# Kernel optimization log

Measured on AMD Instinct MI355X. Metric: run time of the kernel, lower is better.

The kernel has to match this reference:

```python
import jax, jax.numpy as jnp
import numpy as np

N = 50000
E = 800000
IN_FEATS = 128
OUT_FEATS = 16
EDGE_FEATS = 1
NUM_HEADS = 8


def setup_inputs() -> dict:
    key = jax.random.key(0)
    ks = jax.random.split(key, 8)

    def xavier(k, shape):
        fan_in, fan_out = shape[-1], shape[-2] if len(shape) > 1 else shape[-1]
        bound = float(np.sqrt(6.0 / (shape[0] + shape[1])))
        return jax.random.uniform(k, shape, jnp.float32, -bound, bound)

    h = jax.random.normal(ks[0], (N, IN_FEATS), jnp.float32)
    edge_index = jax.random.randint(ks[1], (2, E), 0, N, jnp.int32)
    edge_feat = jax.random.normal(ks[2], (E, EDGE_FEATS), jnp.float32)
    # W_node stored as [in_feats, out_feats*num_heads] so h @ W_node == torch Linear(h)
    W_node = xavier(ks[3], (IN_FEATS, OUT_FEATS * NUM_HEADS))
    W_edge = xavier(ks[4], (EDGE_FEATS, NUM_HEADS))
    a_src = xavier(ks[5], (NUM_HEADS, OUT_FEATS))
    a_dst = xavier(ks[6], (NUM_HEADS, OUT_FEATS))
    return {"h": h, "edge_index": edge_index, "edge_feat": edge_feat,
            "W_node": W_node, "W_edge": W_edge, "a_src": a_src, "a_dst": a_dst}


def reference(h, edge_index, edge_feat, W_node, W_edge, a_src, a_dst):
    n = h.shape[0]
    src, dst = edge_index[0], edge_index[1]
    # node projection: [N, H, F]
    h_trans = (h @ W_node).reshape(n, NUM_HEADS, OUT_FEATS)
    # edge projection: [E, H]
    e_trans = edge_feat @ W_edge
    src_feat = h_trans[src]  # [E, H, F]
    dst_feat = h_trans[dst]  # [E, H, F]
    attn = (src_feat * a_src).sum(-1) + (dst_feat * a_dst).sum(-1) + e_trans  # [E, H]
    attn = jax.nn.leaky_relu(attn, negative_slope=0.2)
    # segment softmax over edges grouped by dst
    max_val = jax.ops.segment_max(attn, dst, num_segments=n)  # [N, H]
    exp_attn = jnp.exp(attn - max_val[dst])
    sum_exp = jax.ops.segment_sum(exp_attn, dst, num_segments=n)  # [N, H]
    alpha = exp_attn / jnp.maximum(sum_exp[dst], 1e-12)  # [E, H]
    msg = src_feat * alpha[..., None]  # [E, H, F]
    out = jax.ops.segment_sum(msg, dst, num_segments=n)  # [N, H, F]
    return out.mean(axis=1)  # [N, F]
```

## Files before the change

### kernel.cpp

```cpp
#include <hip/hip_runtime.h>

#define N_NODES 50000
#define N_EDGES 800000
#define IN_F    128
#define HEADS   8
#define OUT_F   16

typedef unsigned short u16;
typedef __attribute__((ext_vector_type(8))) short bf16x8;
typedef __attribute__((ext_vector_type(4))) float f32x4;

__device__ __forceinline__ float bf2f(u16 u) {
    return __uint_as_float(((unsigned)u) << 16);
}
__device__ __forceinline__ u16 f2bf(float f) {
    unsigned u = __float_as_uint(f);
    unsigned r = 0x7fffu + ((u >> 16) & 1u);
    return (u16)((u + r) >> 16);
}
__device__ __forceinline__ float ldf(const void* p, int i, bool bf) {
    return bf ? bf2f(((const u16*)p)[i]) : ((const float*)p)[i];
}

__global__ void probe_dtype(const void* __restrict__ h, int* __restrict__ flag) {
    if (threadIdx.x == 0 && blockIdx.x == 0) {
        const u16* u = (const u16*)h;
        int cnt = 0;
        for (int i = 0; i < 128; ++i) {
            int e = (u[i] >> 7) & 0xFF;
            if (e >= 90 && e <= 141) cnt++;
        }
        *flag = (cnt >= 110) ? 1 : 0;
    }
}

__global__ __launch_bounds__(256) void init_bufs(float* __restrict__ sum_exp,
                                                 float* __restrict__ out_acc) {
    int i = blockIdx.x * 256 + threadIdx.x;
    if (i < N_NODES * HEADS)  sum_exp[i] = 0.0f;
    if (i < N_NODES * OUT_F)  out_acc[i] = 0.0f;
}

#define WT_STRIDE 136
__global__ __launch_bounds__(256) void node_proj_mfma(
    const void* __restrict__ h, const void* __restrict__ Wn,
    const void* __restrict__ a_srcp, const void* __restrict__ a_dstp,
    const int* __restrict__ flag,
    u16* __restrict__ ht, float* __restrict__ s_src, float* __restrict__ s_dst)
{
    const bool bf = (*flag) != 0;
    __shared__ u16 Wsh[IN_F * WT_STRIDE];
    const int tid = threadIdx.x;

    for (int i = tid; i < IN_F * IN_F; i += 256) {
        int k = i >> 7, c = i & 127;
        u16 v = bf ? ((const u16*)Wn)[i] : f2bf(((const float*)Wn)[i]);
        Wsh[c * WT_STRIDE + k] = v;
    }
    __syncthreads();

    const int wave = tid >> 6, lane = tid & 63;
    const int m = lane & 15, q = lane >> 4;
    const int row_t = blockIdx.x * 64 + wave * 16;

    bf16x8 afr[4];
    int arow = row_t + m;
    if (arow >= N_NODES) arow = N_NODES - 1;
    if (bf) {
        const u16* hp = (const u16*)h + (size_t)arow * IN_F;
        #pragma unroll
        for (int kt = 0; kt < 4; ++kt)
            afr[kt] = *(const bf16x8*)(hp + kt * 32 + q * 8);
    } else {
        const float* hp = (const float*)h + (size_t)arow * IN_F;
        #pragma unroll
        for (int kt = 0; kt < 4; ++kt) {
            bf16x8 t;
            #pragma unroll
            for (int j = 0; j < 8; ++j) t[j] = (short)f2bf(hp[kt * 32 + q * 8 + j]);
            afr[kt] = t;
        }
    }

    for (int ct = 0; ct < 8; ++ct) {
        f32x4 acc = {0.f, 0.f, 0.f, 0.f};
        #pragma unroll
        for (int kt = 0; kt < 4; ++kt) {
            bf16x8 bfr = *(const bf16x8*)(Wsh + (ct * 16 + m) * WT_STRIDE + kt * 32 + q * 8);
            acc = __builtin_amdgcn_mfma_f32_16x16x32_bf16(afr[kt], bfr, acc, 0, 0, 0);
        }
        const float asv = ldf(a_srcp, ct * 16 + m, bf);
        const float adv = ldf(a_dstp, ct * 16 + m, bf);
        float v1[4], v2[4];
        #pragma unroll
        for (int r = 0; r < 4; ++r) {
            int grow = row_t + q * 4 + r;
            if (grow < N_NODES)
                ht[(size_t)grow * IN_F + ct * 16 + m] = f2bf(acc[r]);
            v1[r] = acc[r] * asv;
            v2[r] = acc[r] * adv;
        }
        #pragma unroll
        for (int o = 1; o < 16; o <<= 1) {
            #pragma unroll
            for (int r = 0; r < 4; ++r) {
                v1[r] += __shfl_xor(v1[r], o, 16);
                v2[r] += __shfl_xor(v2[r], o, 16);
            }
        }
        if (m == 0) {
            #pragma unroll
            for (int r = 0; r < 4; ++r) {
                int grow = row_t + q * 4 + r;
                if (grow < N_NODES) {
                    s_src[grow * HEADS + ct] = v1[r];
                    s_dst[grow * HEADS + ct] = v2[r];
                }
            }
        }
    }
}

__device__ __forceinline__ float edge_attn(const int* ei, const void* ef,
                                           const void* We,
                                           const float* s_src, const float* s_dst,
                                           int e, int hh, bool bf,
                                           int& src, int& dst) {
    src = ei[e];
    dst = ei[N_EDGES + e];
    float a = s_src[src * HEADS + hh] + s_dst[dst * HEADS + hh]
            + ldf(ef, e, bf) * ldf(We, hh, bf);
    return (a > 0.0f) ? a : 0.2f * a;
}

__global__ __launch_bounds__(256) void edge_sum(
    const int* __restrict__ ei, const void* __restrict__ ef,
    const void* __restrict__ We, const int* __restrict__ flag,
    const float* __restrict__ s_src, const float* __restrict__ s_dst,
    float* __restrict__ sum_exp)
{
    const bool bf = (*flag) != 0;
    int t = blockIdx.x * 256 + threadIdx.x;
    if (t >= N_EDGES * HEADS) return;
    int e = t >> 3, hh = t & 7, src, dst;
    float a = edge_attn(ei, ef, We, s_src, s_dst, e, hh, bf, src, dst);
    atomicAdd(&sum_exp[dst * HEADS + hh], __expf(a));
}

__global__ __launch_bounds__(256) void edge_aggregate(
    const int* __restrict__ ei, const void* __restrict__ ef,
    const void* __restrict__ We, const int* __restrict__ flag,
    const float* __restrict__ s_src, const float* __restrict__ s_dst,
    const float* __restrict__ sum_exp,
    const u16* __restrict__ ht, float* __restrict__ out_acc)
{
    const bool bf = (*flag) != 0;
    int t = blockIdx.x * 256 + threadIdx.x;
    int e = t >> 4;
    if (e >= N_EDGES) return;
    int lane = threadIdx.x & 15;
    int hh = lane & 7, src, dst;
    float a = edge_attn(ei, ef, We, s_src, s_dst, e, hh, bf, src, dst);
    float alpha = __expf(a) / fmaxf(sum_exp[dst * HEADS + hh], 1e-12f);

    const u16* hp = ht + (size_t)src * IN_F + lane;
    float acc = 0.0f;
    #pragma unroll
    for (int h2 = 0; h2 < HEADS; ++h2) {
        float ah = __shfl(alpha, h2, 16);
        acc = fmaf(ah, bf2f(hp[h2 * 16]), acc);
    }
    atomicAdd(&out_acc[dst * OUT_F + lane], acc * 0.125f);
}

__global__ __launch_bounds__(256) void finalize(const float* __restrict__ out_acc,
                                                void* __restrict__ out,
                                                const int* __restrict__ flag) {
    const bool bf = (*flag) != 0;
    int i = blockIdx.x * 256 + threadIdx.x;
    if (i < N_NODES * OUT_F) {
        float v = out_acc[i];
        if (bf) ((u16*)out)[i] = f2bf(v);
        else    ((float*)out)[i] = v;
    }
}

extern "C" void kernel_launch(void* const* d_in, const int* in_sizes, int n_in,
                              void* d_out, int out_size, void* d_ws, size_t ws_size,
                              hipStream_t stream) {
    const void* h     = d_in[0];
    const int*  ei    = (const int*)d_in[1];
    const void* efeat = d_in[2];
    const void* Wn    = d_in[3];
    const void* We    = d_in[4];
    const void* a_src = d_in[5];
    const void* a_dst = d_in[6];

    char* ws = (char*)d_ws;
    int*   flag    = (int*)ws;   ws += 256;
    u16*   ht      = (u16*)ws;   ws += (size_t)N_NODES * IN_F * 2;
    float* s_src   = (float*)ws; ws += (size_t)N_NODES * HEADS * 4;
    float* s_dst   = (float*)ws; ws += (size_t)N_NODES * HEADS * 4;
    float* sum_exp = (float*)ws; ws += (size_t)N_NODES * HEADS * 4;
    float* out_acc = (float*)ws; ws += (size_t)N_NODES * OUT_F * 4;

    hipLaunchKernelGGL(probe_dtype, dim3(1), dim3(64), 0, stream, h, flag);
    hipLaunchKernelGGL(init_bufs, dim3((N_NODES * OUT_F + 255) / 256), dim3(256),
                       0, stream, sum_exp, out_acc);
    hipLaunchKernelGGL(node_proj_mfma, dim3((N_NODES + 63) / 64), dim3(256),
                       0, stream, h, Wn, a_src, a_dst, flag, ht, s_src, s_dst);
    hipLaunchKernelGGL(edge_sum, dim3((N_EDGES * HEADS + 255) / 256), dim3(256),
                       0, stream, ei, efeat, We, flag, s_src, s_dst, sum_exp);
    hipLaunchKernelGGL(edge_aggregate, dim3((N_EDGES * 16 + 255) / 256), dim3(256),
                       0, stream, ei, efeat, We, flag, s_src, s_dst, sum_exp,
                       ht, out_acc);
    hipLaunchKernelGGL(finalize, dim3((N_NODES * OUT_F + 255) / 256), dim3(256),
                       0, stream, out_acc, d_out, flag);
}
```

Baseline: 225.1 us.

## Transpose ht layout to feature-major for vectorized loads; one thread per edge in edge_sum

The projected node features are now stored per row with the 8 heads of each output feature packed together (index f*8+head), written as one 16-byte vector per row. edge_aggregate then reads a single 16-byte vector per lane instead of eight strided 2-byte loads. edge_sum assigns one thread per edge, loading the src/dst scores with float4 and issuing eight atomics, instead of one thread per (edge, head). This cuts the number of gather transactions and repeated index loads, but edge_sum now has fewer threads, each doing serialized atomics.

```diff
diff --git a/kernel.cpp b/kernel.cpp
--- a/kernel.cpp
+++ b/kernel.cpp
@@ -82,6 +82,8 @@
         }
     }
 
+    f32x4 accs[8];
+    #pragma unroll
     for (int ct = 0; ct < 8; ++ct) {
         f32x4 acc = {0.f, 0.f, 0.f, 0.f};
         #pragma unroll
@@ -89,14 +91,12 @@
             bf16x8 bfr = *(const bf16x8*)(Wsh + (ct * 16 + m) * WT_STRIDE + kt * 32 + q * 8);
             acc = __builtin_amdgcn_mfma_f32_16x16x32_bf16(afr[kt], bfr, acc, 0, 0, 0);
         }
+        accs[ct] = acc;
         const float asv = ldf(a_srcp, ct * 16 + m, bf);
         const float adv = ldf(a_dstp, ct * 16 + m, bf);
         float v1[4], v2[4];
         #pragma unroll
         for (int r = 0; r < 4; ++r) {
-            int grow = row_t + q * 4 + r;
-            if (grow < N_NODES)
-                ht[(size_t)grow * IN_F + ct * 16 + m] = f2bf(acc[r]);
             v1[r] = acc[r] * asv;
             v2[r] = acc[r] * adv;
         }
@@ -119,18 +119,17 @@
             }
         }
     }
-}
-
-__device__ __forceinline__ float edge_attn(const int* ei, const void* ef,
-                                           const void* We,
-                                           const float* s_src, const float* s_dst,
-                                           int e, int hh, bool bf,
-                                           int& src, int& dst) {
-    src = ei[e];
-    dst = ei[N_EDGES + e];
-    float a = s_src[src * HEADS + hh] + s_dst[dst * HEADS + hh]
-            + ldf(ef, e, bf) * ldf(We, hh, bf);
-    return (a > 0.0f) ? a : 0.2f * a;
+
+    #pragma unroll
+    for (int r = 0; r < 4; ++r) {
+        int grow = row_t + q * 4 + r;
+        if (grow < N_NODES) {
+            bf16x8 o;
+            #pragma unroll
+            for (int ct = 0; ct < 8; ++ct) o[ct] = (short)f2bf(accs[ct][r]);
+            *(bf16x8*)(ht + (size_t)grow * IN_F + m * 8) = o;
+        }
+    }
 }
 
 __global__ __launch_bounds__(256) void edge_sum(
@@ -140,11 +139,24 @@
     float* __restrict__ sum_exp)
 {
     const bool bf = (*flag) != 0;
-    int t = blockIdx.x * 256 + threadIdx.x;
-    if (t >= N_EDGES * HEADS) return;
-    int e = t >> 3, hh = t & 7, src, dst;
-    float a = edge_attn(ei, ef, We, s_src, s_dst, e, hh, bf, src, dst);
-    atomicAdd(&sum_exp[dst * HEADS + hh], __expf(a));
+    int e = blockIdx.x * 256 + threadIdx.x;
+    if (e >= N_EDGES) return;
+    int src = ei[e];
+    int dst = ei[N_EDGES + e];
+    const float4* sp = (const float4*)(s_src + src * HEADS);
+    const float4* dp = (const float4*)(s_dst + dst * HEADS);
+    float4 sa = sp[0], sb = sp[1];
+    float4 da = dp[0], db = dp[1];
+    float efv = ldf(ef, e, bf);
+    float s8[8] = {sa.x, sa.y, sa.z, sa.w, sb.x, sb.y, sb.z, sb.w};
+    float d8[8] = {da.x, da.y, da.z, da.w, db.x, db.y, db.z, db.w};
+    float* se = sum_exp + dst * HEADS;
+    #pragma unroll
+    for (int hh = 0; hh < 8; ++hh) {
+        float a = s8[hh] + d8[hh] + efv * ldf(We, hh, bf);
+        a = (a > 0.0f) ? a : 0.2f * a;
+        atomicAdd(&se[hh], __expf(a));
+    }
 }
 
 __global__ __launch_bounds__(256) void edge_aggregate(
@@ -159,16 +171,23 @@
     int e = t >> 4;
     if (e >= N_EDGES) return;
     int lane = threadIdx.x & 15;
-    int hh = lane & 7, src, dst;
-    float a = edge_attn(ei, ef, We, s_src, s_dst, e, hh, bf, src, dst);
-    float alpha = __expf(a) / fmaxf(sum_exp[dst * HEADS + hh], 1e-12f);
-
-    const u16* hp = ht + (size_t)src * IN_F + lane;
+    int src = ei[e];
+    int dst = ei[N_EDGES + e];
+
+    float alpha = 0.0f;
+    if (lane < 8) {
+        float a = s_src[src * HEADS + lane] + s_dst[dst * HEADS + lane]
+                + ldf(ef, e, bf) * ldf(We, lane, bf);
+        a = (a > 0.0f) ? a : 0.2f * a;
+        alpha = __expf(a) / fmaxf(sum_exp[dst * HEADS + lane], 1e-12f);
+    }
+
+    bf16x8 v = *(const bf16x8*)(ht + (size_t)src * IN_F + lane * 8);
     float acc = 0.0f;
     #pragma unroll
     for (int h2 = 0; h2 < HEADS; ++h2) {
         float ah = __shfl(alpha, h2, 16);
-        acc = fmaf(ah, bf2f(hp[h2 * 16]), acc);
+        acc = fmaf(ah, bf2f((u16)v[h2]), acc);
     }
     atomicAdd(&out_acc[dst * OUT_F + lane], acc * 0.125f);
 }
@@ -209,7 +228,7 @@
                        0, stream, sum_exp, out_acc);
     hipLaunchKernelGGL(node_proj_mfma, dim3((N_NODES + 63) / 64), dim3(256),
                        0, stream, h, Wn, a_src, a_dst, flag, ht, s_src, s_dst);
-    hipLaunchKernelGGL(edge_sum, dim3((N_EDGES * HEADS + 255) / 256), dim3(256),
+    hipLaunchKernelGGL(edge_sum, dim3((N_EDGES + 255) / 256), dim3(256),
                        0, stream, ei, efeat, We, flag, s_src, s_dst, sum_exp);
     hipLaunchKernelGGL(edge_aggregate, dim3((N_EDGES * 16 + 255) / 256), dim3(256),
                        0, stream, ei, efeat, We, flag, s_src, s_dst, sum_exp,
```

Measured after the change: 512.4 us. 128% more time.

## Store projected features feature-major so edge gather uses one 16-byte load per lane

Applied to the files above, without the earlier changes.

The node projection now keeps all eight head accumulators and writes each node row of ht as [feature][head], packing the eight heads of a feature into one 16-byte store. The aggregation kernel then reads those eight head values with a single vector load per lane instead of eight strided 2-byte loads. Only the first eight lanes of each edge compute the attention score and alpha, which removes redundant gathers of s_src, s_dst and sum_exp. The cost is more live registers in the projection kernel to hold the accumulators.

```diff
diff --git a/kernel.cpp b/kernel.cpp
--- a/kernel.cpp
+++ b/kernel.cpp
@@ -82,6 +82,8 @@
         }
     }
 
+    f32x4 accs[8];
+    #pragma unroll
     for (int ct = 0; ct < 8; ++ct) {
         f32x4 acc = {0.f, 0.f, 0.f, 0.f};
         #pragma unroll
@@ -89,14 +91,12 @@
             bf16x8 bfr = *(const bf16x8*)(Wsh + (ct * 16 + m) * WT_STRIDE + kt * 32 + q * 8);
             acc = __builtin_amdgcn_mfma_f32_16x16x32_bf16(afr[kt], bfr, acc, 0, 0, 0);
         }
+        accs[ct] = acc;
         const float asv = ldf(a_srcp, ct * 16 + m, bf);
         const float adv = ldf(a_dstp, ct * 16 + m, bf);
         float v1[4], v2[4];
         #pragma unroll
         for (int r = 0; r < 4; ++r) {
-            int grow = row_t + q * 4 + r;
-            if (grow < N_NODES)
-                ht[(size_t)grow * IN_F + ct * 16 + m] = f2bf(acc[r]);
             v1[r] = acc[r] * asv;
             v2[r] = acc[r] * adv;
         }
@@ -117,6 +117,17 @@
                     s_dst[grow * HEADS + ct] = v2[r];
                 }
             }
+        }
+    }
+
+    #pragma unroll
+    for (int r = 0; r < 4; ++r) {
+        int grow = row_t + q * 4 + r;
+        if (grow < N_NODES) {
+            bf16x8 o;
+            #pragma unroll
+            for (int ct = 0; ct < 8; ++ct) o[ct] = (short)f2bf(accs[ct][r]);
+            *(bf16x8*)(ht + (size_t)grow * IN_F + m * 8) = o;
         }
     }
 }
@@ -159,16 +170,23 @@
     int e = t >> 4;
     if (e >= N_EDGES) return;
     int lane = threadIdx.x & 15;
-    int hh = lane & 7, src, dst;
-    float a = edge_attn(ei, ef, We, s_src, s_dst, e, hh, bf, src, dst);
-    float alpha = __expf(a) / fmaxf(sum_exp[dst * HEADS + hh], 1e-12f);
-
-    const u16* hp = ht + (size_t)src * IN_F + lane;
+    int src = ei[e];
+    int dst = ei[N_EDGES + e];
+
+    float alpha = 0.0f;
+    if (lane < 8) {
+        float a = s_src[src * HEADS + lane] + s_dst[dst * HEADS + lane]
+                + ldf(ef, e, bf) * ldf(We, lane, bf);
+        a = (a > 0.0f) ? a : 0.2f * a;
+        alpha = __expf(a) / fmaxf(sum_exp[dst * HEADS + lane], 1e-12f);
+    }
+
+    bf16x8 v = *(const bf16x8*)(ht + (size_t)src * IN_F + lane * 8);
     float acc = 0.0f;
     #pragma unroll
     for (int h2 = 0; h2 < HEADS; ++h2) {
         float ah = __shfl(alpha, h2, 16);
-        acc = fmaf(ah, bf2f(hp[h2 * 16]), acc);
+        acc = fmaf(ah, bf2f((u16)v[h2]), acc);
     }
     atomicAdd(&out_acc[dst * OUT_F + lane], acc * 0.125f);
 }
```

Measured after the change: 227.1 us. About the same (+0.9%).
